# Optimization experiments

Hardware: AMD Instinct MI355X
Metric: run time of the kernel (lower is better)

The kernel has to match this reference:

```python
import jax, jax.numpy as jnp
import numpy as np

N_ACT = 3  # [relu, tanh, sigmoid]


def setup_inputs() -> dict:
    key = jax.random.key(0)
    k1, k2, k3 = jax.random.split(key, 3)
    B, IN, OUT = 4096, 4096, 4096
    x = jax.random.normal(k1, (B, IN), dtype=jnp.float32)
    W = jax.random.normal(k2, (OUT, IN), dtype=jnp.float32)
    b = jax.random.normal(k3, (OUT,), dtype=jnp.float32)
    return {"x": x, "W": W, "b": b}


def reference(x, W, b):
    # Linear: y = x @ W^T + b  -> [B, OUT]
    y = jnp.einsum("bi,oi->bo", x, W) + b
    # Per-output-column criterion: mean over batch, then idx = int(mean % 3).
    # torch `%` on tensors is remainder with the divisor's sign (non-negative
    # here), and int() then truncates == floor for non-negative values.
    means = jnp.mean(y, axis=0)                        # [OUT]
    idx = jnp.mod(means, float(N_ACT)).astype(jnp.int32)  # [OUT] in {0,1,2}
    idx_b = idx[None, :]                               # broadcast over batch
    # Device-side branchless select among the three activations.
    out = jnp.where(
        idx_b == 0,
        jax.nn.relu(y),
        jnp.where(idx_b == 1, jnp.tanh(y), jax.nn.sigmoid(y)),
    )
    return out
```

## Files before the change

### kernel.cpp

```cpp
#include <hip/hip_runtime.h>
#include <hip/hip_bf16.h>
#include <math.h>

#define B_DIM   4096
#define IN_DIM  4096
#define OUT_DIM 4096

typedef __attribute__((ext_vector_type(8))) short  short8;
typedef __attribute__((ext_vector_type(4))) float  floatx4;

__device__ __forceinline__ ushort f2bf(float f) {
    unsigned b = __float_as_uint(f);
    return (ushort)((b + 0x7fffu + ((b >> 16) & 1u)) >> 16);
}

__global__ void cvt_x_colsum(const float* __restrict__ x, ushort* __restrict__ xb,
                             double* __restrict__ part) {
    int c0 = blockIdx.x * 1024 + threadIdx.x * 4;
    int r0 = blockIdx.y * 16;
    double s0 = 0, s1 = 0, s2 = 0, s3 = 0;
#pragma unroll 4
    for (int r = 0; r < 16; ++r) {
        size_t off = (size_t)(r0 + r) * IN_DIM + c0;
        float4 v = *(const float4*)(x + off);
        ushort4 o;
        o.x = f2bf(v.x); o.y = f2bf(v.y); o.z = f2bf(v.z); o.w = f2bf(v.w);
        *(ushort4*)(xb + off) = o;
        s0 += (double)v.x; s1 += (double)v.y; s2 += (double)v.z; s3 += (double)v.w;
    }
    double* p = part + (size_t)blockIdx.y * IN_DIM + c0;
    p[0] = s0; p[1] = s1; p[2] = s2; p[3] = s3;
}

__global__ void xbar_reduce(const double* __restrict__ part, double* __restrict__ xbar) {
    __shared__ double red[256];
    int col   = blockIdx.x * 64 + (threadIdx.x & 63);
    int slice = threadIdx.x >> 6;
    double s = 0.0;
    for (int rb = slice * 64; rb < slice * 64 + 64; ++rb)
        s += part[(size_t)rb * IN_DIM + col];
    red[threadIdx.x] = s;
    __syncthreads();
    if (slice == 0) {
        double v = red[threadIdx.x] + red[threadIdx.x + 64]
                 + red[threadIdx.x + 128] + red[threadIdx.x + 192];
        xbar[col] = v * (1.0 / (double)B_DIM);
    }
}

__global__ void cvt_w_means(const float* __restrict__ W, const float* __restrict__ bias,
                            const double* __restrict__ xbar, ushort* __restrict__ wb,
                            int* __restrict__ idx) {
    __shared__ double red[256];
    int o = blockIdx.x;
    size_t base = (size_t)o * IN_DIM;
    double s = 0.0;
#pragma unroll
    for (int j = 0; j < 4; ++j) {
        int i = j * 1024 + threadIdx.x * 4;
        float4 v = *(const float4*)(W + base + i);
        ushort4 ob;
        ob.x = f2bf(v.x); ob.y = f2bf(v.y); ob.z = f2bf(v.z); ob.w = f2bf(v.w);
        *(ushort4*)(wb + base + i) = ob;
        double2 xv0 = *(const double2*)(xbar + i);
        double2 xv1 = *(const double2*)(xbar + i + 2);
        s += (double)v.x * xv0.x + (double)v.y * xv0.y
           + (double)v.z * xv1.x + (double)v.w * xv1.y;
    }
    red[threadIdx.x] = s;
    __syncthreads();
    for (int st = 128; st > 0; st >>= 1) {
        if (threadIdx.x < st) red[threadIdx.x] += red[threadIdx.x + st];
        __syncthreads();
    }
    if (threadIdx.x == 0) {
        float mf = (float)(red[0] + (double)bias[o]);
        float md = fmodf(mf, 3.0f);
        if (md < 0.0f) md += 3.0f;
        idx[o] = (int)md;
    }
}

__global__ void __launch_bounds__(256) gemm_bt_act(
    const ushort* __restrict__ A,
    const ushort* __restrict__ Bt,
    const float*  __restrict__ bias,
    const int*    __restrict__ idx,
    float*        __restrict__ out) {
    __shared__ __align__(16) ushort As[128 * 64];
    __shared__ __align__(16) ushort Bs[128 * 64];

    const int t    = threadIdx.x;
    const int w    = t >> 6;
    const int l    = t & 63;
    const int quad = l >> 4;
    const int lrow = l & 15;

    const int b   = blockIdx.y * 32 + blockIdx.x;
    const int sup = b >> 6;
    const int q   = b & 63;
    const int m0  = ((sup >> 2) * 8 + (q >> 3)) * 128;
    const int n0  = ((sup & 3)  * 8 + (q & 7))  * 128;

    const int m0w  = (w >> 1) * 64;
    const int n0w  = (w & 1) * 64;
    const int K    = IN_DIM;

    floatx4 acc[4][4] = {};

    for (int k0 = 0; k0 < K; k0 += 64) {
#pragma unroll
        for (int j = 0; j < 4; ++j) {
            int chunk = j * 256 + t;
            int r     = chunk >> 3;
            int kb    = (chunk & 7) ^ (r & 7);
            int goff  = kb << 3;
            int ldsoff = (j * 256 + w * 64) * 8;
            __builtin_amdgcn_global_load_lds(
                (__attribute__((address_space(1))) void*)(A + (size_t)(m0 + r) * K + k0 + goff),
                (__attribute__((address_space(3))) void*)(As + ldsoff), 16, 0, 0);
            __builtin_amdgcn_global_load_lds(
                (__attribute__((address_space(1))) void*)(Bt + (size_t)(n0 + r) * K + k0 + goff),
                (__attribute__((address_space(3))) void*)(Bs + ldsoff), 16, 0, 0);
        }
        __syncthreads();

#pragma unroll
        for (int s = 0; s < 2; ++s) {
            short8 af[4], bf[4];
#pragma unroll
            for (int mi = 0; mi < 4; ++mi) {
                int r = m0w + mi * 16 + lrow;
                int kb = (s * 4 + quad) ^ (r & 7);
                af[mi] = *(const short8*)&As[r * 64 + kb * 8];
            }
#pragma unroll
            for (int ni = 0; ni < 4; ++ni) {
                int r = n0w + ni * 16 + lrow;
                int kb = (s * 4 + quad) ^ (r & 7);
                bf[ni] = *(const short8*)&Bs[r * 64 + kb * 8];
            }
#pragma unroll
            for (int mi = 0; mi < 4; ++mi)
#pragma unroll
                for (int ni = 0; ni < 4; ++ni)
                    acc[mi][ni] = __builtin_amdgcn_mfma_f32_16x16x32_bf16(
                        af[mi], bf[ni], acc[mi][ni], 0, 0, 0);
        }
        __syncthreads();
    }

#pragma unroll
    for (int ni = 0; ni < 4; ++ni) {
        int   col     = n0 + n0w + ni * 16 + lrow;
        int   id      = idx[col];
        float bv      = bias[col];
        float a       = (id == 1) ? -2.0f : -1.0f;
        bool  isrelu  = (id == 0);
        bool  istanh  = (id == 1);
#pragma unroll
        for (int mi = 0; mi < 4; ++mi) {
            int rowb = m0 + m0w + mi * 16 + quad * 4;
#pragma unroll
            for (int r = 0; r < 4; ++r) {
                float y   = acc[mi][ni][r] + bv;
                float e   = __expf(a * y);
                float s   = __builtin_amdgcn_rcpf(1.0f + e);
                float act = istanh ? fmaf(2.0f, s, -1.0f) : s;
                float v   = isrelu ? fmaxf(y, 0.0f) : act;
                out[(size_t)(rowb + r) * OUT_DIM + col] = v;
            }
        }
    }
}

extern "C" void kernel_launch(void* const* d_in, const int* in_sizes, int n_in,
                              void* d_out, int out_size, void* d_ws, size_t ws_size,
                              hipStream_t stream) {
    const float* x = (const float*)d_in[0];
    const float* W = (const float*)d_in[1];
    const float* b = (const float*)d_in[2];
    float* out = (float*)d_out;

    char* ws = (char*)d_ws;
    ushort* xb   = (ushort*)(ws);
    ushort* wb   = (ushort*)(ws + (33554432));
    double* part = (double*)(ws + (67108864));
    double* xbar = (double*)(ws + (67108864 + 8388608));
    int*    idx  = (int*)   (ws + (67108864 + 8388608 + 32768));

    cvt_x_colsum<<<dim3(4, 256), 256, 0, stream>>>(x, xb, part);
    xbar_reduce<<<64, 256, 0, stream>>>(part, xbar);
    cvt_w_means<<<4096, 256, 0, stream>>>(W, b, xbar, wb, idx);
    gemm_bt_act<<<dim3(32, 32), 256, 0, stream>>>(xb, wb, b, idx, out);
}
```

Measured before the change: 351.4 us.

## Restructure GEMM to 256x256 tiles with 4-stage async LDS pipeline

Rewrites the bf16 GEMM kernel to use 256x256 output tiles with 512 threads (8 waves, 128x64 per wave) and a 4-slot ring buffer of K=32 stages filled by global_load_lds. This replaces the old single-buffered load/sync/compute loop. The K loop issues loads three stages ahead, waits with an explicit vmcnt, and raises wave priority around the MFMA block. The grid becomes 256 blocks mapped with an XCD-aware swizzle. Risks are higher register pressure from 32 accumulators per wave, a single wave of blocks across the CUs, and the hand-tuned waitcnt being correct only for this load count.

```diff
diff --git a/kernel.cpp b/kernel.cpp
--- a/kernel.cpp
+++ b/kernel.cpp
@@ -81,86 +81,113 @@
     }
 }
 
-__global__ void __launch_bounds__(256) gemm_bt_act(
+__global__ void __launch_bounds__(512, 2) gemm_bt_act(
     const ushort* __restrict__ A,
     const ushort* __restrict__ Bt,
     const float*  __restrict__ bias,
     const int*    __restrict__ idx,
     float*        __restrict__ out) {
-    __shared__ __align__(16) ushort As[128 * 64];
-    __shared__ __align__(16) ushort Bs[128 * 64];
+    __shared__ __align__(16) ushort lds[4][2][256 * 32];
 
     const int t    = threadIdx.x;
     const int w    = t >> 6;
     const int l    = t & 63;
     const int quad = l >> 4;
     const int lrow = l & 15;
-
-    const int b   = blockIdx.y * 32 + blockIdx.x;
-    const int sup = b >> 6;
-    const int q   = b & 63;
-    const int m0  = ((sup >> 2) * 8 + (q >> 3)) * 128;
-    const int n0  = ((sup & 3)  * 8 + (q & 7))  * 128;
-
-    const int m0w  = (w >> 1) * 64;
-    const int n0w  = (w & 1) * 64;
-    const int K    = IN_DIM;
-
-    floatx4 acc[4][4] = {};
-
-    for (int k0 = 0; k0 < K; k0 += 64) {
-#pragma unroll
-        for (int j = 0; j < 4; ++j) {
-            int chunk = j * 256 + t;
-            int r     = chunk >> 3;
-            int kb    = (chunk & 7) ^ (r & 7);
-            int goff  = kb << 3;
-            int ldsoff = (j * 256 + w * 64) * 8;
+    const int wm   = w >> 2;
+    const int wn   = w & 3;
+
+    const int b   = blockIdx.x;
+    const int xcd = b & 7;
+    const int p   = b >> 3;
+    const int m0  = ((xcd >> 1) * 4 + (p >> 3)) * 256;
+    const int n0  = ((xcd & 1) * 8 + (p & 7)) * 256;
+
+    const int K = IN_DIM;
+
+    size_t aoff[2], boff[2];
+    int    ldso[2];
+#pragma unroll
+    for (int j = 0; j < 2; ++j) {
+        int chunk = j * 512 + t;
+        int r     = chunk >> 2;
+        int kb    = (chunk & 3) ^ ((r >> 1) & 3);
+        aoff[j] = (size_t)(m0 + r) * K + kb * 8;
+        boff[j] = (size_t)(n0 + r) * K + kb * 8;
+        ldso[j] = chunk * 8;
+    }
+
+    const int kbsw  = (quad ^ ((lrow >> 1) & 3)) * 16;
+    const int abase = (wm * 128 + lrow) * 64 + kbsw;
+    const int bbase = (wn * 64 + lrow) * 64 + kbsw;
+
+    floatx4 acc[8][4] = {};
+
+#pragma unroll
+    for (int pt = 0; pt < 3; ++pt) {
+        int ks = pt * 32;
+#pragma unroll
+        for (int j = 0; j < 2; ++j) {
             __builtin_amdgcn_global_load_lds(
-                (__attribute__((address_space(1))) void*)(A + (size_t)(m0 + r) * K + k0 + goff),
-                (__attribute__((address_space(3))) void*)(As + ldsoff), 16, 0, 0);
+                (__attribute__((address_space(1))) void*)(A + aoff[j] + ks),
+                (__attribute__((address_space(3))) void*)(&lds[pt][0][ldso[j]]), 16, 0, 0);
             __builtin_amdgcn_global_load_lds(
-                (__attribute__((address_space(1))) void*)(Bt + (size_t)(n0 + r) * K + k0 + goff),
-                (__attribute__((address_space(3))) void*)(Bs + ldsoff), 16, 0, 0);
+                (__attribute__((address_space(1))) void*)(Bt + boff[j] + ks),
+                (__attribute__((address_space(3))) void*)(&lds[pt][1][ldso[j]]), 16, 0, 0);
         }
-        __syncthreads();
-
-#pragma unroll
-        for (int s = 0; s < 2; ++s) {
-            short8 af[4], bf[4];
-#pragma unroll
-            for (int mi = 0; mi < 4; ++mi) {
-                int r = m0w + mi * 16 + lrow;
-                int kb = (s * 4 + quad) ^ (r & 7);
-                af[mi] = *(const short8*)&As[r * 64 + kb * 8];
+    }
+
+#pragma unroll 1
+    for (int kt = 0; kt < 128; ++kt) {
+        asm volatile("s_waitcnt vmcnt(8)" ::: "memory");
+        __builtin_amdgcn_s_barrier();
+
+        {
+            int nt   = (kt + 3) & 127;
+            int slot = (kt + 3) & 3;
+            int ks   = nt * 32;
+#pragma unroll
+            for (int j = 0; j < 2; ++j) {
+                __builtin_amdgcn_global_load_lds(
+                    (__attribute__((address_space(1))) void*)(A + aoff[j] + ks),
+                    (__attribute__((address_space(3))) void*)(&lds[slot][0][ldso[j]]), 16, 0, 0);
+                __builtin_amdgcn_global_load_lds(
+                    (__attribute__((address_space(1))) void*)(Bt + boff[j] + ks),
+                    (__attribute__((address_space(3))) void*)(&lds[slot][1][ldso[j]]), 16, 0, 0);
             }
-#pragma unroll
-            for (int ni = 0; ni < 4; ++ni) {
-                int r = n0w + ni * 16 + lrow;
-                int kb = (s * 4 + quad) ^ (r & 7);
-                bf[ni] = *(const short8*)&Bs[r * 64 + kb * 8];
-            }
-#pragma unroll
-            for (int mi = 0; mi < 4; ++mi)
-#pragma unroll
-                for (int ni = 0; ni < 4; ++ni)
-                    acc[mi][ni] = __builtin_amdgcn_mfma_f32_16x16x32_bf16(
-                        af[mi], bf[ni], acc[mi][ni], 0, 0, 0);
         }
-        __syncthreads();
+
+        const char* sa = (const char*)&lds[kt & 3][0][0];
+        const char* sb = (const char*)&lds[kt & 3][1][0];
+        short8 af[8], bf[4];
+#pragma unroll
+        for (int mi = 0; mi < 8; ++mi)
+            af[mi] = *(const short8*)(sa + abase + mi * 1024);
+#pragma unroll
+        for (int ni = 0; ni < 4; ++ni)
+            bf[ni] = *(const short8*)(sb + bbase + ni * 1024);
+
+        __builtin_amdgcn_s_setprio(1);
+#pragma unroll
+        for (int mi = 0; mi < 8; ++mi)
+#pragma unroll
+            for (int ni = 0; ni < 4; ++ni)
+                acc[mi][ni] = __builtin_amdgcn_mfma_f32_16x16x32_bf16(
+                    af[mi], bf[ni], acc[mi][ni], 0, 0, 0);
+        __builtin_amdgcn_s_setprio(0);
     }
 
 #pragma unroll
     for (int ni = 0; ni < 4; ++ni) {
-        int   col     = n0 + n0w + ni * 16 + lrow;
+        int   col     = n0 + wn * 64 + ni * 16 + lrow;
         int   id      = idx[col];
         float bv      = bias[col];
         float a       = (id == 1) ? -2.0f : -1.0f;
         bool  isrelu  = (id == 0);
         bool  istanh  = (id == 1);
 #pragma unroll
-        for (int mi = 0; mi < 4; ++mi) {
-            int rowb = m0 + m0w + mi * 16 + quad * 4;
+        for (int mi = 0; mi < 8; ++mi) {
+            int rowb = m0 + wm * 128 + mi * 16 + quad * 4;
 #pragma unroll
             for (int r = 0; r < 4; ++r) {
                 float y   = acc[mi][ni][r] + bv;
@@ -192,5 +219,5 @@
     cvt_x_colsum<<<dim3(4, 256), 256, 0, stream>>>(x, xb, part);
     xbar_reduce<<<64, 256, 0, stream>>>(part, xbar);
     cvt_w_means<<<4096, 256, 0, stream>>>(W, b, xbar, wb, idx);
-    gemm_bt_act<<<dim3(32, 32), 256, 0, stream>>>(xb, wb, b, idx, out);
-}
+    gemm_bt_act<<<256, 512, 0, stream>>>(xb, wb, b, idx, out);
+}
```

New measurement: 322.4 us. 1.09x faster.
